# Kernel optimization log

Hardware: AMD Instinct MI355X
Metric: run time of the kernel (lower is better)

Reference implementation:

```python
import jax, jax.numpy as jnp
import numpy as np

BATCH, SEQ, DIM = 4, 4096, 256
DT_RANK, D_STATE, NUM_TOKENS = 16, 16, 1024


def _adapool(x, T):
    # uniform window mean == AdaptiveAvgPool1d when S % T == 0
    B, S, D = x.shape
    return x.reshape(B, T, S // T, D).mean(axis=2)


def _layernorm(x, g, b, eps=1e-5):
    mu = x.mean(-1, keepdims=True)
    var = ((x - mu) ** 2).mean(-1, keepdims=True)
    return (x - mu) * jax.lax.rsqrt(var + eps) * g + b


def _gauss_mask(T):
    c = (T + 1) // 2
    idx = jnp.arange(T, dtype=jnp.float32)
    sigma = jnp.abs(idx - c).mean()
    w = jnp.exp(-0.5 * (idx - c) ** 2 / sigma ** 2)
    return w / w.sum()


def _ssm(x, Wdbc, Wdt, bdt, Alog, D):
    A = -jnp.exp(Alog)                                     # (Dm, N)
    dbc = x @ Wdbc.T                                       # (B,L,dt+2N)
    delta = jax.nn.softplus(dbc[..., :DT_RANK] @ Wdt.T + bdt)   # (B,L,Dm)
    Bm = dbc[..., DT_RANK:DT_RANK + D_STATE]               # (B,L,N)
    Cm = dbc[..., DT_RANK + D_STATE:]                      # (B,L,N)
    deltaA = jnp.exp(delta[..., None] * A)                 # (B,L,Dm,N)
    BX = (delta[..., None] * Bm[:, :, None, :]) * x[..., None]
    def comb(c1, c2):
        a1, x1 = c1
        a2, x2 = c2
        return (a2 * a1, a2 * x1 + x2)
    _, hs = jax.lax.associative_scan(comb, (deltaA, BX), axis=1)
    y = jnp.einsum('bldn,bln->bld', hs, Cm) + D * x
    return y


def setup_inputs():
    key = jax.random.key(0)
    ks = jax.random.split(key, 16)
    s = 0.05
    Alog = jnp.tile(jnp.log(jnp.arange(1.0, D_STATE + 1.0, dtype=jnp.float32))[None, :], (DIM, 1))
    return {
        'x': jax.random.normal(ks[0], (BATCH, SEQ, DIM), jnp.float32),
        'ln_g': jnp.ones((DIM,), jnp.float32),
        'ln_b': jnp.zeros((DIM,), jnp.float32),
        'W1': jax.random.normal(ks[1], (DIM, DIM), jnp.float32) * s,
        'b1': jnp.zeros((DIM,), jnp.float32),
        'W2': jax.random.normal(ks[2], (DIM, DIM), jnp.float32) * s,
        'b2': jnp.zeros((DIM,), jnp.float32),
        'Wcf': jax.random.normal(ks[3], (DIM, DIM), jnp.float32) * s,
        'bcf': jnp.zeros((DIM,), jnp.float32),
        'Wcb': jax.random.normal(ks[4], (DIM, DIM), jnp.float32) * s,
        'bcb': jnp.zeros((DIM,), jnp.float32),
        'Wdbc_f': jax.random.normal(ks[5], (DT_RANK + 2 * D_STATE, DIM), jnp.float32) * s,
        'Wdt_f': jax.random.normal(ks[6], (DIM, DT_RANK), jnp.float32) * s,
        'bdt_f': jnp.zeros((DIM,), jnp.float32),
        'Alog_f': Alog,
        'D_f': jnp.ones((DIM,), jnp.float32),
        'Wdbc_b': jax.random.normal(ks[7], (DT_RANK + 2 * D_STATE, DIM), jnp.float32) * s,
        'Wdt_b': jax.random.normal(ks[8], (DIM, DT_RANK), jnp.float32) * s,
        'bdt_b': jnp.zeros((DIM,), jnp.float32),
        'Alog_b': Alog,
        'D_b': jnp.ones((DIM,), jnp.float32),
    }


def reference(x, ln_g, ln_b, W1, b1, W2, b2, Wcf, bcf, Wcb, bcb,
              Wdbc_f, Wdt_f, bdt_f, Alog_f, D_f,
              Wdbc_b, Wdt_b, bdt_b, Alog_b, D_b):
    skip = _adapool(x, NUM_TOKENS)
    xn = _layernorm(x, ln_g, ln_b)
    z = xn @ W1.T + b1
    xp = xn @ W2.T + b2
    mask = _gauss_mask(NUM_TOKENS)[None, :, None]

    # forward direction: 1x1 conv (= channel linear) -> softplus -> SSM
    h1 = jax.nn.softplus(jnp.einsum('bsd,ed->bse', xp, Wcf) + bcf)
    x1 = _ssm(h1, Wdbc_f, Wdt_f, bdt_f, Alog_f, D_f)
    x1 = jax.nn.silu(_adapool(x1, NUM_TOKENS) * mask)

    # backward direction on flipped sequence
    h2 = jax.nn.softplus(jnp.einsum('bsd,ed->bse', xp[:, ::-1], Wcb) + bcb)
    x2 = _ssm(h2, Wdbc_b, Wdt_b, bdt_b, Alog_b, D_b)[:, ::-1]
    x2 = jax.nn.silu(_adapool(x2, NUM_TOKENS) * mask)

    zp = jax.nn.silu(_adapool(z, NUM_TOKENS))
    return zp * x1 + zp * x2 + skip
```

## Files before the change

### kernel.cpp

```cpp
#include <hip/hip_runtime.h>
#include <math.h>


namespace {
constexpr int BB = 4;
constexpr int LL = 4096;
constexpr int DD = 256;
constexpr int NS = 16;
constexpr int NCH = 128;
constexpr int CLEN = 32;
constexpr int NG  = CLEN / 8;
constexpr int TOK = 1024;

constexpr size_t NROW = (size_t)BB * LL;
constexpr size_t NE   = NROW * DD;
constexpr size_t NP   = (size_t)BB * TOK * DD;
constexpr size_t NBC  = NROW * NS;
constexpr size_t NAGG = 2ull * BB * DD * NCH * NS;
constexpr size_t NSD  = 2ull * BB * NCH * DD;

constexpr size_t O_H1X  = 0;
constexpr size_t O_G2X  = NE / 2;
constexpr size_t O_H1T  = NE;
constexpr size_t O_G2T  = NE + NE / 2;
constexpr size_t O_DLTF = 2 * NE;
constexpr size_t O_XN   = O_DLTF;
constexpr size_t O_DLTB = 2 * NE + NE / 2;
constexpr size_t O_BMF  = 3 * NE;
constexpr size_t O_CMF  = O_BMF + NBC / 2;
constexpr size_t O_BMB  = O_CMF + NBC / 2;
constexpr size_t O_CMB  = O_BMB + NBC / 2;
constexpr size_t O_ZP   = O_CMB + NBC / 2;
constexpr size_t O_WF1  = O_ZP + NP;
constexpr size_t O_BF1  = O_WF1 + 768 * 256 / 2;
constexpr size_t O_WF2F = O_BF1 + 768;
constexpr size_t O_B2F  = O_WF2F + 384 * 256 / 2;
constexpr size_t O_WF2B = O_B2F + 384;
constexpr size_t O_B2B  = O_WF2B + 384 * 256 / 2;
constexpr size_t O_SD   = O_B2B + 384;
constexpr size_t O_HEND = O_SD + NSD;
constexpr size_t O_HIN  = O_HEND + NAGG / 2;
constexpr size_t O_MASK = O_HIN + NAGG / 2;

constexpr int SST = 136;
}

typedef __bf16 bf16x8 __attribute__((ext_vector_type(8)));
typedef __bf16 bf16x4 __attribute__((ext_vector_type(4)));
typedef float f32x4 __attribute__((ext_vector_type(4)));

__device__ __forceinline__ float softplusf(float x) {
    return fmaxf(x, 0.f) + __logf(1.f + __expf(-fabsf(x)));
}
__device__ __forceinline__ float siluf(float x) {
    return x / (1.f + __expf(-x));
}
__device__ __forceinline__ void gl_lds16(const void* g, void* l) {
    __builtin_amdgcn_global_load_lds((const __attribute__((address_space(1))) unsigned int*)g,
                                     (__attribute__((address_space(3))) unsigned int*)l, 16, 0, 0);
}
__device__ __forceinline__ int st_addr(int col, int row) {
    return col * SST + ((((row >> 3) ^ (col >> 3)) & 15) << 3) + (row & 7);
}
__device__ __forceinline__ void pow_chain(float e1, float* p) {
    p[0] = e1;
    p[1] = e1 * e1;
    p[2] = p[1] * e1;
    p[3] = p[1] * p[1];
    p[4] = p[3] * p[0];
    p[5] = p[3] * p[1];
    p[6] = p[3] * p[2];
    p[7] = p[3] * p[3];
    p[8]  = p[7] * p[0];
    p[9]  = p[7] * p[1];
    p[10] = p[7] * p[2];
    p[11] = p[7] * p[3];
    p[12] = p[7] * p[4];
    p[13] = p[7] * p[5];
    p[14] = p[7] * p[6];
    p[15] = p[7] * p[7];
}

#define GEMM_KLOOP(SHBASE, GA, GB, WR, WC, WV, LANE, ACC)                          \
    {                                                                               \
        _Pragma("unroll")                                                           \
        for (int rg = 0; rg < 2; ++rg) {                                            \
            gl_lds16((GA) + rg * 16 * 256, &(SHBASE)[((WV) * 2 + rg) * 512]);       \
            gl_lds16((GB) + rg * 16 * 256, &(SHBASE)[4096 + ((WV) * 2 + rg) * 512]);\
        }                                                                           \
        _Pragma("unroll")                                                           \
        for (int kst = 0; kst < 8; ++kst) {                                         \
            if (kst < 7) {                                                          \
                __bf16* Asn = (SHBASE) + ((kst + 1) & 1) * 8192;                    \
                int k0n = (kst + 1) * 32;                                           \
                _Pragma("unroll")                                                   \
                for (int rg = 0; rg < 2; ++rg) {                                    \
                    gl_lds16((GA) + rg * 16 * 256 + k0n, &Asn[((WV) * 2 + rg) * 512]);      \
                    gl_lds16((GB) + rg * 16 * 256 + k0n, &Asn[4096 + ((WV) * 2 + rg) * 512]);\
                }                                                                   \
                asm volatile("s_waitcnt vmcnt(4)" ::: "memory");                    \
            } else {                                                                \
                asm volatile("s_waitcnt vmcnt(0)" ::: "memory");                    \
            }                                                                       \
            __builtin_amdgcn_s_barrier();                                           \
            __builtin_amdgcn_sched_barrier(0);                                      \
            const __bf16* Ac = (SHBASE) + (kst & 1) * 8192;                         \
            const __bf16* Bc = Ac + 4096;                                           \
            bf16x8 af[4], bfr[4];                                                   \
            _Pragma("unroll")                                                       \
            for (int i = 0; i < 4; ++i)                                             \
                af[i] = *(const bf16x8*)&Ac[((WR) * 4 + i) * 512 + (LANE) * 8];     \
            _Pragma("unroll")                                                       \
            for (int j = 0; j < 4; ++j)                                             \
                bfr[j] = *(const bf16x8*)&Bc[((WC) * 4 + j) * 512 + (LANE) * 8];    \
            _Pragma("unroll")                                                       \
            for (int i = 0; i < 4; ++i)                                             \
                _Pragma("unroll")                                                   \
                for (int j = 0; j < 4; ++j)                                         \
                    ACC[i][j] = __builtin_amdgcn_mfma_f32_16x16x32_bf16(af[i], bfr[j], ACC[i][j], 0, 0, 0); \
            __builtin_amdgcn_s_barrier();                                           \
        }                                                                           \
    }

__global__ __launch_bounds__(256) void prep_ln_kernel(
    const float* __restrict__ x, const float* __restrict__ lng, const float* __restrict__ lnb,
    const float* __restrict__ W1, const float* __restrict__ b1,
    const float* __restrict__ W2, const float* __restrict__ b2,
    const float* __restrict__ Wcf, const float* __restrict__ bcf,
    const float* __restrict__ Wcb, const float* __restrict__ bcb,
    const float* __restrict__ Wdt_f, const float* __restrict__ Wdbc_f, const float* __restrict__ bdt_f,
    const float* __restrict__ Wdt_b, const float* __restrict__ Wdbc_b, const float* __restrict__ bdt_b,
    __bf16* __restrict__ xn, float* __restrict__ outp,
    __bf16* __restrict__ Wf1, float* __restrict__ bf1,
    __bf16* __restrict__ Wf2f, float* __restrict__ b2f,
    __bf16* __restrict__ Wf2b, float* __restrict__ b2b,
    float* __restrict__ mask)
{
    int bxg = blockIdx.x;
    int k = threadIdx.x;
    if (bxg < 4096) {
        __shared__ float red[32];
        __shared__ float mv[8];
        int t = k;
        int r0 = bxg * 4;
        float gg = lng[t], bbv = lnb[t];
        float v[4], s[4], q[4];
#pragma unroll
        for (int i = 0; i < 4; ++i) {
            v[i] = x[(size_t)(r0 + i) * 256 + t];
            s[i] = v[i];
            q[i] = v[i] * v[i];
        }
        for (int o = 32; o > 0; o >>= 1) {
#pragma unroll
            for (int i = 0; i < 4; ++i) {
                s[i] += __shfl_xor(s[i], o, 64);
                q[i] += __shfl_xor(q[i], o, 64);
            }
        }
        if ((t & 63) == 0) {
            int w = t >> 6;
#pragma unroll
            for (int i = 0; i < 4; ++i) { red[i * 4 + w] = s[i]; red[16 + i * 4 + w] = q[i]; }
        }
        __syncthreads();
        if (t < 4) {
            float S = red[t * 4 + 0] + red[t * 4 + 1] + red[t * 4 + 2] + red[t * 4 + 3];
            float Q = red[16 + t * 4 + 0] + red[16 + t * 4 + 1] + red[16 + t * 4 + 2] + red[16 + t * 4 + 3];
            float mu = S * (1.f / 256.f);
            mv[t * 2] = mu;
            mv[t * 2 + 1] = rsqrtf(Q * (1.f / 256.f) - mu * mu + 1e-5f);
        }
        __syncthreads();
        float acc = 0.f;
#pragma unroll
        for (int i = 0; i < 4; ++i) {
            xn[(size_t)(r0 + i) * 256 + t] = (__bf16)((v[i] - mv[i * 2]) * mv[i * 2 + 1] * gg + bbv);
            acc += v[i];
        }
        int b = r0 >> 12;
        int g = (r0 & 4095) >> 2;
        outp[((size_t)b * TOK + g) * 256 + t] = acc * 0.25f;
        return;
    }
    int j2 = bxg - 4096;
    int mat = j2 / 641;
    int bx = j2 % 641;
    if (bx < 256) {
        int j = bx;
        const float* Wc = mat ? Wcb : Wcf;
        float acc = 0.f, accb = 0.f;
#pragma unroll 8
        for (int m = 0; m < 256; ++m) {
            float w = Wc[j * 256 + m];
            acc  = fmaf(w, W2[m * 256 + k], acc);
            accb = fmaf(w, b2[m], accb);
        }
        Wf1[(size_t)(256 + mat * 256 + j) * 256 + k] = (__bf16)acc;
        if (k == 0) bf1[256 + mat * 256 + j] = accb + (mat ? bcb[j] : bcf[j]);
        if (mat == 0) {
            Wf1[(size_t)j * 256 + k] = (__bf16)W1[j * 256 + k];
            if (k == 0) bf1[j] = b1[j];
        }
    } else if (bx < 640) {
        int j = bx - 256;
        const float* Wdt  = mat ? Wdt_b : Wdt_f;
        const float* Wdbc = mat ? Wdbc_b : Wdbc_f;
        const float* bdt  = mat ? bdt_b : bdt_f;
        __bf16* Wf2 = mat ? Wf2b : Wf2f;
        float* b2x  = mat ? b2b : b2f;
        float val;
        if (j < 256) {
            float acc = 0.f;
#pragma unroll
            for (int m = 0; m < 16; ++m)
                acc = fmaf(Wdt[j * 16 + m], Wdbc[m * 256 + k], acc);
            val = acc;
        } else if (j < 288) {
            val = Wdbc[(16 + (j - 256)) * 256 + k];
        } else {
            val = 0.f;
        }
        Wf2[(size_t)j * 256 + k] = (__bf16)val;
        if (k == 0) b2x[j] = (j < 256) ? bdt[j] : 0.f;
    } else if (mat == 0) {
        __shared__ float red2[4];
        __shared__ float sb;
        float w[4];
        float loc = 0.f;
#pragma unroll
        for (int q = 0; q < 4; ++q) {
            float dd = (float)(k + 256 * q) - 512.f;
            w[q] = __expf(-0.5f * dd * dd * (1.f / 65536.f));
            loc += w[q];
        }
        for (int o = 32; o > 0; o >>= 1) loc += __shfl_xor(loc, o, 64);
        if ((k & 63) == 0) red2[k >> 6] = loc;
        __syncthreads();
        if (k == 0) sb = red2[0] + red2[1] + red2[2] + red2[3];
        __syncthreads();
        float inv = 1.f / sb;
#pragma unroll
        for (int q = 0; q < 4; ++q) mask[k + 256 * q] = w[q] * inv;
    }
}

__global__ __launch_bounds__(256) void gemm1_mfma(
    const __bf16* __restrict__ A, const __bf16* __restrict__ Bw, const float* __restrict__ bias,
    float* __restrict__ zp, __bf16* __restrict__ h1x, __bf16* __restrict__ g2x,
    __bf16* __restrict__ h1T, __bf16* __restrict__ g2T)
{
    __shared__ __align__(16) __bf16 SH[128 * SST];
    int tid = threadIdx.x;
    int lane = tid & 63, wv = tid >> 6;
    int wr = wv >> 1, wc = wv & 1;
    int lm = lane & 15, lq = lane >> 4;
    int m0 = blockIdx.x << 7, n0 = blockIdx.y << 7;

    const __bf16* gaB = A  + (size_t)(m0 + wv * 32 + lm) * 256 + lq * 8;
    const __bf16* gbB = Bw + (size_t)(n0 + wv * 32 + lm) * 256 + lq * 8;

    f32x4 acc[4][4];
#pragma unroll
    for (int i = 0; i < 4; ++i)
#pragma unroll
        for (int j = 0; j < 4; ++j) acc[i][j] = 0;

    GEMM_KLOOP(SH, gaB, gbB, wr, wc, wv, lane, acc)

    int target = blockIdx.y >> 1;
    int colbase = (blockIdx.y & 1) * 128;
    __syncthreads();
    if (target == 0) {
        float* zs = (float*)SH;
#pragma unroll
        for (int j = 0; j < 4; ++j) {
            int coll = wc * 64 + j * 16 + lm;
            float bv = bias[n0 + coll];
#pragma unroll
            for (int i = 0; i < 4; ++i) {
                int gl = wr * 16 + i * 4 + lq;
                float s = acc[i][j][0] + acc[i][j][1] + acc[i][j][2] + acc[i][j][3];
                zs[gl * 132 + coll] = siluf(0.25f * s + bv);
            }
        }
        __syncthreads();
        int b = m0 >> 12, g0 = (m0 & 4095) >> 2;
        int rl = tid >> 5;
        int c4 = (tid & 31) * 4;
#pragma unroll
        for (int p = 0; p < 4; ++p) {
            int g = p * 8 + rl;
            float4 v = *(float4*)&zs[g * 132 + c4];
            *(float4*)&zp[((size_t)b * TOK + g0 + g) * 256 + colbase + c4] = v;
        }
    } else {
        __bf16* hs = SH;
#pragma unroll
        for (int j = 0; j < 4; ++j) {
            int coll = wc * 64 + j * 16 + lm;
            float bv = bias[n0 + coll];
#pragma unroll
            for (int i = 0; i < 4; ++i) {
                int rl = wr * 64 + i * 16 + lq * 4;
                bf16x4 v4;
#pragma unroll
                for (int r = 0; r < 4; ++r)
                    v4[r] = (__bf16)softplusf(acc[i][j][r] + bv);
                *(bf16x4*)&hs[st_addr(coll, rl)] = v4;
            }
        }
        __syncthreads();
        __bf16* outp = (target == 1) ? h1x : g2x;
        __bf16* outT = (target == 1) ? h1T : g2T;
        {
            int tg = tid >> 4;
#pragma unroll
            for (int it = 0; it < 8; ++it) {
                int dcol = it * 16 + (tid & 15);
                bf16x8 v = *(const bf16x8*)&hs[dcol * SST + (((tg ^ (dcol >> 3)) & 15) << 3)];
                *(bf16x8*)&outT[(((size_t)(m0 >> 3) + tg) * 256 + colbase + dcol) * 8] = v;
            }
        }
        {
            int rl2 = tid >> 4;
            int c8 = (tid & 15) * 8;
#pragma unroll
            for (int p = 0; p < 8; ++p) {
                int row = p * 16 + rl2;
                bf16x8 v;
#pragma unroll
                for (int e = 0; e < 8; ++e) v[e] = hs[st_addr(c8 + e, row)];
                *(bf16x8*)&outp[(size_t)(m0 + row) * 256 + colbase + c8] = v;
            }
        }
    }
}

__global__ __launch_bounds__(256) void gemm2_mfma(
    const __bf16* __restrict__ h1x, const __bf16* __restrict__ g2x,
    const __bf16* __restrict__ Wf, const float* __restrict__ bf2,
    const __bf16* __restrict__ Wb, const float* __restrict__ bb2,
    __bf16* __restrict__ dTf, __bf16* __restrict__ dTb,
    __bf16* __restrict__ BmF, __bf16* __restrict__ CmF,
    __bf16* __restrict__ BmB, __bf16* __restrict__ CmB)
{
    __shared__ __align__(16) __bf16 SH[128 * SST];
    int tid = threadIdx.x;
    int lane = tid & 63, wv = tid >> 6;
    int wr = wv >> 1, wc = wv & 1;
    int lm = lane & 15, lq = lane >> 4;
    int m0 = blockIdx.x << 7, n0 = blockIdx.y << 7;
    int dir = blockIdx.z;
    const __bf16* A    = dir ? g2x : h1x;
    const __bf16* Bw   = dir ? Wb : Wf;
    const float* bias  = dir ? bb2 : bf2;
    __bf16* dT = dir ? dTb : dTf;
    __bf16* Bm = dir ? BmB : BmF;
    __bf16* Cm = dir ? CmB : CmF;

    const __bf16* gaB = A  + (size_t)(m0 + wv * 32 + lm) * 256 + lq * 8;
    const __bf16* gbB = Bw + (size_t)(n0 + wv * 32 + lm) * 256 + lq * 8;

    f32x4 acc[4][4];
#pragma unroll
    for (int i = 0; i < 4; ++i)
#pragma unroll
        for (int j = 0; j < 4; ++j) acc[i][j] = 0;

    GEMM_KLOOP(SH, gaB, gbB, wr, wc, wv, lane, acc)

    __syncthreads();
    if (blockIdx.y < 2) {
        __bf16* hs = SH;
        int colbase = blockIdx.y * 128;
#pragma unroll
        for (int j = 0; j < 4; ++j) {
            int coll = wc * 64 + j * 16 + lm;
            float bv = bias[n0 + coll];
#pragma unroll
            for (int i = 0; i < 4; ++i) {
                int rl = wr * 64 + i * 16 + lq * 4;
                bf16x4 v4;
#pragma unroll
                for (int r = 0; r < 4; ++r)
                    v4[r] = (__bf16)softplusf(acc[i][j][r] + bv);
                *(bf16x4*)&hs[st_addr(coll, rl)] = v4;
            }
        }
        __syncthreads();
        int tg = tid >> 4;
#pragma unroll
        for (int it = 0; it < 8; ++it) {
            int dcol = it * 16 + (tid & 15);
            bf16x8 v = *(const bf16x8*)&hs[dcol * SST + (((tg ^ (dcol >> 3)) & 15) << 3)];
            *(bf16x8*)&dT[(((size_t)(m0 >> 3) + tg) * 256 + colbase + dcol) * 8] = v;
        }
    } else {
        __bf16* bs_ = SH;
        __bf16* cs_ = SH + 128 * 24;
        if (wc == 0) {
#pragma unroll
            for (int j = 0; j < 2; ++j) {
                int coll = j * 16 + lm;
                float bv = bias[n0 + coll];
                __bf16* dst = j ? cs_ : bs_;
#pragma unroll
                for (int i = 0; i < 4; ++i) {
                    int rl = wr * 64 + i * 16 + lq * 4;
#pragma unroll
                    for (int r = 0; r < 4; ++r)
                        dst[(rl + r) * 24 + lm] = (__bf16)(acc[i][j][r] + bv);
                }
            }
        }
        __syncthreads();
        int row = tid >> 1;
        int c8 = (tid & 1) * 8;
        bf16x8 vb = *(bf16x8*)&bs_[row * 24 + c8];
        bf16x8 vc = *(bf16x8*)&cs_[row * 24 + c8];
        *(bf16x8*)&Bm[(size_t)(m0 + row) * 16 + c8] = vb;
        *(bf16x8*)&Cm[(size_t)(m0 + row) * 16 + c8] = vc;
    }
}

__global__ __launch_bounds__(256) void scan1_kernel(
    const __bf16* __restrict__ dTf, const __bf16* __restrict__ dTb,
    const __bf16* __restrict__ xTf, const __bf16* __restrict__ xTb,
    const __bf16* __restrict__ bmf, const __bf16* __restrict__ bmb,
    const float* __restrict__ alogf, const float* __restrict__ alogb,
    float* __restrict__ sdb, __bf16* __restrict__ hend)
{
    int d = threadIdx.x;
    int c = blockIdx.x, b = blockIdx.y, dir = blockIdx.z;
    const __bf16* dT = dir ? dTb : dTf;
    const __bf16* xT = dir ? xTb : xTf;
    const __bf16* Bm = dir ? bmb : bmf;
    const float* Alog = dir ? alogb : alogf;

    float A[16];
    bool intOK = true;
#pragma unroll
    for (int n = 0; n < 16; ++n) {
        A[n] = -__expf(Alog[(size_t)d * 16 + n]);
        intOK = intOK && (fabsf(A[n] + (float)(n + 1)) < 1e-3f);
    }
    float h[16];
#pragma unroll
    for (int n = 0; n < 16; ++n) h[n] = 0.f;
    float sd = 0.f;
    size_t rg0 = (size_t)b * 512 + (size_t)c * NG;
    size_t rowb = (size_t)b * LL + (size_t)c * CLEN;
    if (intOK) {
        for (int g = 0; g < NG; ++g) {
            int gg = dir ? (NG - 1 - g) : g;
            size_t ti = ((rg0 + gg) * 256 + d) * 8;
            bf16x8 dv = *(const bf16x8*)&dT[ti];
            bf16x8 xv8 = *(const bf16x8*)&xT[ti];
#pragma unroll
            for (int ii = 0; ii < 8; ++ii) {
                int i = dir ? (7 - ii) : ii;
                float dlt = (float)dv[i];
                float xv  = (float)xv8[i];
                float common = dlt * xv;
                sd += dlt;
                float p[16];
                pow_chain(__expf(-dlt), p);
                const bf16x8* Bp = (const bf16x8*)&Bm[(rowb + gg * 8 + i) * NS];
                bf16x8 b0 = Bp[0], b1 = Bp[1];
#pragma unroll
                for (int n = 0; n < 8; ++n) {
                    h[n]     = fmaf(p[n],     h[n],     common * (float)b0[n]);
                    h[n + 8] = fmaf(p[n + 8], h[n + 8], common * (float)b1[n]);
                }
            }
        }
    } else {
        for (int g = 0; g < NG; ++g) {
            int gg = dir ? (NG - 1 - g) : g;
            size_t ti = ((rg0 + gg) * 256 + d) * 8;
            bf16x8 dv = *(const bf16x8*)&dT[ti];
            bf16x8 xv8 = *(const bf16x8*)&xT[ti];
#pragma unroll
            for (int ii = 0; ii < 8; ++ii) {
                int i = dir ? (7 - ii) : ii;
                float dlt = (float)dv[i];
                float xv  = (float)xv8[i];
                float common = dlt * xv;
                sd += dlt;
                const bf16x8* Bp = (const bf16x8*)&Bm[(rowb + gg * 8 + i) * NS];
                bf16x8 b0 = Bp[0], b1 = Bp[1];
#pragma unroll
                for (int n = 0; n < 8; ++n) {
                    h[n]     = fmaf(__expf(dlt * A[n]),     h[n],     common * (float)b0[n]);
                    h[n + 8] = fmaf(__expf(dlt * A[n + 8]), h[n + 8], common * (float)b1[n]);
                }
            }
        }
    }
    size_t sbase = (size_t)(dir * 4 + b) * NCH + c;
    sdb[sbase * 256 + d] = sd;
    size_t hb = sbase * 16 * 256 + d;
#pragma unroll
    for (int n = 0; n < 16; ++n) hend[hb + (size_t)n * 256] = (__bf16)h[n];
}

__global__ __launch_bounds__(128) void scan2_kernel(
    const float* __restrict__ sdb, const __bf16* __restrict__ hend,
    const float* __restrict__ alogf, const float* __restrict__ alogb,
    __bf16* __restrict__ hin)
{
    int blk = blockIdx.x >> 1;
    int n = blk & 15, b = (blk >> 4) & 3, dir = blk >> 6;
    int d = ((blockIdx.x & 1) << 7) + threadIdx.x;
    const float* Alog = dir ? alogb : alogf;
    float A_dn = -__expf(Alog[(size_t)d * 16 + n]);
    size_t basec = (size_t)(dir * 4 + b) * NCH;
    float s = 0.f;
    if (!dir) {
#pragma unroll 8
        for (int c = 0; c < NCH; ++c) {
            float sdv = sdb[(basec + c) * 256 + d];
            size_t idx = ((basec + c) * 16 + n) * 256 + d;
            float he = (float)hend[idx];
            hin[idx] = (__bf16)s;
            s = fmaf(__expf(sdv * A_dn), s, he);
        }
    } else {
#pragma unroll 8
        for (int c = NCH - 1; c >= 0; --c) {
            float sdv = sdb[(basec + c) * 256 + d];
            size_t idx = ((basec + c) * 16 + n) * 256 + d;
            float he = (float)hend[idx];
            hin[idx] = (__bf16)s;
            s = fmaf(__expf(sdv * A_dn), s, he);
        }
    }
}

__global__ __launch_bounds__(256) void scan3_kernel(
    const __bf16* __restrict__ dTf, const __bf16* __restrict__ dTb,
    const __bf16* __restrict__ xTf, const __bf16* __restrict__ xTb,
    const __bf16* __restrict__ bmf, const __bf16* __restrict__ bmb,
    const __bf16* __restrict__ cmf, const __bf16* __restrict__ cmb,
    const float* __restrict__ alogf, const float* __restrict__ alogb,
    const float* __restrict__ Dfp, const float* __restrict__ Dbp,
    const __bf16* __restrict__ hin,
    const float* __restrict__ zp, const float* __restrict__ mask,
    float* __restrict__ outp)
{
    int d = threadIdx.x;
    int c = blockIdx.x, b = blockIdx.y, dir = blockIdx.z;
    const __bf16* dT = dir ? dTb : dTf;
    const __bf16* xT = dir ? xTb : xTf;
    const __bf16* Bm = dir ? bmb : bmf;
    const __bf16* Cm = dir ? cmb : cmf;
    const float* Alog = dir ? alogb : alogf;
    const float* Dv   = dir ? Dbp : Dfp;

    float A[16];
    bool intOK = true;
#pragma unroll
    for (int n = 0; n < 16; ++n) {
        A[n] = -__expf(Alog[(size_t)d * 16 + n]);
        intOK = intOK && (fabsf(A[n] + (float)(n + 1)) < 1e-3f);
    }
    float Dd = Dv[d];
    float h[16];
    size_t hb = ((size_t)(dir * 4 + b) * NCH + c) * 16 * 256 + d;
#pragma unroll
    for (int n = 0; n < 16; ++n) h[n] = (float)hin[hb + (size_t)n * 256];

    size_t rg0 = (size_t)b * 512 + (size_t)c * NG;
    size_t rowb = (size_t)b * LL + (size_t)c * CLEN;
    int base = c * CLEN;
    float pool = 0.f;
    if (intOK) {
        for (int g = 0; g < NG; ++g) {
            int gg = dir ? (NG - 1 - g) : g;
            size_t ti = ((rg0 + gg) * 256 + d) * 8;
            bf16x8 dv = *(const bf16x8*)&dT[ti];
            bf16x8 xv8 = *(const bf16x8*)&xT[ti];
#pragma unroll
            for (int ii = 0; ii < 8; ++ii) {
                int i = dir ? (7 - ii) : ii;
                float dlt = (float)dv[i];
                float xv  = (float)xv8[i];
                float common = dlt * xv;
                float p[16];
                pow_chain(__expf(-dlt), p);
                size_t row = rowb + gg * 8 + i;
                const bf16x8* Bp = (const bf16x8*)&Bm[row * NS];
                const bf16x8* Cp = (const bf16x8*)&Cm[row * NS];
                bf16x8 b0 = Bp[0], b1 = Bp[1];
                bf16x8 c0 = Cp[0], c1 = Cp[1];
                float yac = 0.f;
#pragma unroll
                for (int n = 0; n < 8; ++n) {
                    h[n]     = fmaf(p[n],     h[n],     common * (float)b0[n]);
                    h[n + 8] = fmaf(p[n + 8], h[n + 8], common * (float)b1[n]);
                    yac = fmaf(h[n], (float)c0[n], yac);
                    yac = fmaf(h[n + 8], (float)c1[n], yac);
                }
                pool += yac + Dd * xv;
                int t = base + gg * 8 + i;
                bool gend = dir ? ((t & 3) == 0) : ((t & 3) == 3);
                if (gend) {
                    int gtok = t >> 2;
                    size_t ip = ((size_t)b * TOK + gtok) * 256 + d;
                    float contrib = zp[ip] * siluf(pool * 0.25f * mask[gtok]);
                    atomicAdd(&outp[ip], contrib);
                    pool = 0.f;
                }
            }
        }
    } else {
        for (int g = 0; g < NG; ++g) {
            int gg = dir ? (NG - 1 - g) : g;
            size_t ti = ((rg0 + gg) * 256 + d) * 8;
            bf16x8 dv = *(const bf16x8*)&dT[ti];
            bf16x8 xv8 = *(const bf16x8*)&xT[ti];
#pragma unroll
            for (int ii = 0; ii < 8; ++ii) {
                int i = dir ? (7 - ii) : ii;
                float dlt = (float)dv[i];
                float xv  = (float)xv8[i];
                float common = dlt * xv;
                size_t row = rowb + gg * 8 + i;
                const bf16x8* Bp = (const bf16x8*)&Bm[row * NS];
                const bf16x8* Cp = (const bf16x8*)&Cm[row * NS];
                bf16x8 b0 = Bp[0], b1 = Bp[1];
                bf16x8 c0 = Cp[0], c1 = Cp[1];
                float yac = 0.f;
#pragma unroll
                for (int n = 0; n < 8; ++n) {
                    h[n]     = fmaf(__expf(dlt * A[n]),     h[n],     common * (float)b0[n]);
                    h[n + 8] = fmaf(__expf(dlt * A[n + 8]), h[n + 8], common * (float)b1[n]);
                    yac = fmaf(h[n], (float)c0[n], yac);
                    yac = fmaf(h[n + 8], (float)c1[n], yac);
                }
                pool += yac + Dd * xv;
                int t = base + gg * 8 + i;
                bool gend = dir ? ((t & 3) == 0) : ((t & 3) == 3);
                if (gend) {
                    int gtok = t >> 2;
                    size_t ip = ((size_t)b * TOK + gtok) * 256 + d;
                    float contrib = zp[ip] * siluf(pool * 0.25f * mask[gtok]);
                    atomicAdd(&outp[ip], contrib);
                    pool = 0.f;
                }
            }
        }
    }
}

extern "C" void kernel_launch(void* const* d_in, const int* in_sizes, int n_in,
                              void* d_out, int out_size, void* d_ws, size_t ws_size,
                              hipStream_t stream)
{
    const float* x      = (const float*)d_in[0];
    const float* ln_g   = (const float*)d_in[1];
    const float* ln_b   = (const float*)d_in[2];
    const float* W1     = (const float*)d_in[3];
    const float* b1     = (const float*)d_in[4];
    const float* W2     = (const float*)d_in[5];
    const float* b2     = (const float*)d_in[6];
    const float* Wcf    = (const float*)d_in[7];
    const float* bcf    = (const float*)d_in[8];
    const float* Wcb    = (const float*)d_in[9];
    const float* bcb    = (const float*)d_in[10];
    const float* Wdbc_f = (const float*)d_in[11];
    const float* Wdt_f  = (const float*)d_in[12];
    const float* bdt_f  = (const float*)d_in[13];
    const float* Alog_f = (const float*)d_in[14];
    const float* D_f    = (const float*)d_in[15];
    const float* Wdbc_b = (const float*)d_in[16];
    const float* Wdt_b  = (const float*)d_in[17];
    const float* bdt_b  = (const float*)d_in[18];
    const float* Alog_b = (const float*)d_in[19];
    const float* D_b    = (const float*)d_in[20];
    float* out = (float*)d_out;
    float* ws  = (float*)d_ws;

    __bf16* h1x = (__bf16*)(ws + O_H1X);
    __bf16* g2x = (__bf16*)(ws + O_G2X);
    __bf16* h1T = (__bf16*)(ws + O_H1T);
    __bf16* g2T = (__bf16*)(ws + O_G2T);
    __bf16* xnb = (__bf16*)(ws + O_XN);
    __bf16* dTf = (__bf16*)(ws + O_DLTF);
    __bf16* dTb = (__bf16*)(ws + O_DLTB);
    __bf16* bmf = (__bf16*)(ws + O_BMF);
    __bf16* cmf = (__bf16*)(ws + O_CMF);
    __bf16* bmb = (__bf16*)(ws + O_BMB);
    __bf16* cmb = (__bf16*)(ws + O_CMB);
    float* zpb  = ws + O_ZP;
    __bf16* wf1 = (__bf16*)(ws + O_WF1);
    float* bf1  = ws + O_BF1;
    __bf16* wf2f = (__bf16*)(ws + O_WF2F);
    float* b2f  = ws + O_B2F;
    __bf16* wf2b = (__bf16*)(ws + O_WF2B);
    float* b2b  = ws + O_B2B;
    float* sdb  = ws + O_SD;
    __bf16* hnd = (__bf16*)(ws + O_HEND);
    __bf16* hin = (__bf16*)(ws + O_HIN);
    float* mkb  = ws + O_MASK;

    prep_ln_kernel<<<dim3(4096 + 1282), 256, 0, stream>>>(
        x, ln_g, ln_b,
        W1, b1, W2, b2, Wcf, bcf, Wcb, bcb,
        Wdt_f, Wdbc_f, bdt_f, Wdt_b, Wdbc_b, bdt_b,
        xnb, out, wf1, bf1, wf2f, b2f, wf2b, b2b, mkb);
    gemm1_mfma<<<dim3(128, 6), 256, 0, stream>>>(xnb, wf1, bf1, zpb, h1x, g2x, h1T, g2T);
    gemm2_mfma<<<dim3(128, 3, 2), 256, 0, stream>>>(h1x, g2x, wf2f, b2f, wf2b, b2b,
                                                    dTf, dTb, bmf, cmf, bmb, cmb);
    scan1_kernel<<<dim3(NCH, BB, 2), 256, 0, stream>>>(dTf, dTb, h1T, g2T, bmf, bmb,
                                                       Alog_f, Alog_b, sdb, hnd);
    scan2_kernel<<<256, 128, 0, stream>>>(sdb, hnd, Alog_f, Alog_b, hin);
    scan3_kernel<<<dim3(NCH, BB, 2), 256, 0, stream>>>(dTf, dTb, h1T, g2T, bmf, bmb, cmf, cmb,
                                                       Alog_f, Alog_b, D_f, D_b, hin,
                                                       zpb, mkb, out);
}
```

Measured before the change: 213.1 us.

## Merge scan3 directions per block and replace atomics with shared-memory reduction

scan3 now runs both scan directions in a single 512-thread block for each chunk. Each thread writes its pooled contribution to shared memory, then one pass adds both directions into the output with plain read-add-write, replacing per-element atomicAdd. Separately, the prep kernel's fused-weight product now computes 8 output rows per block with register accumulation and a warp-shuffle reduction for the bias, which shrinks the grid. The risks are a larger block and shared-memory footprint in scan3, and it only stays correct because each chunk maps to exactly its own 8 tokens.

```diff
diff --git a/kernel.cpp b/kernel.cpp
--- a/kernel.cpp
+++ b/kernel.cpp
@@ -184,26 +184,52 @@
         return;
     }
     int j2 = bxg - 4096;
-    int mat = j2 / 641;
-    int bx = j2 % 641;
-    if (bx < 256) {
-        int j = bx;
-        const float* Wc = mat ? Wcb : Wcf;
-        float acc = 0.f, accb = 0.f;
-#pragma unroll 8
+    int mat = j2 / 417;
+    int bx = j2 % 417;
+    if (bx < 32) {
+        int j0 = bx * 8;
+        const float* Wc  = mat ? Wcb : Wcf;
+        const float* bcx = mat ? bcb : bcf;
+        float b2v = b2[k];
+        float acc[8];
+#pragma unroll
+        for (int jj = 0; jj < 8; ++jj) acc[jj] = 0.f;
+#pragma unroll 4
         for (int m = 0; m < 256; ++m) {
-            float w = Wc[j * 256 + m];
-            acc  = fmaf(w, W2[m * 256 + k], acc);
-            accb = fmaf(w, b2[m], accb);
-        }
-        Wf1[(size_t)(256 + mat * 256 + j) * 256 + k] = (__bf16)acc;
-        if (k == 0) bf1[256 + mat * 256 + j] = accb + (mat ? bcb[j] : bcf[j]);
+            float w2v = W2[m * 256 + k];
+#pragma unroll
+            for (int jj = 0; jj < 8; ++jj)
+                acc[jj] = fmaf(Wc[(j0 + jj) * 256 + m], w2v, acc[jj]);
+        }
+#pragma unroll
+        for (int jj = 0; jj < 8; ++jj)
+            Wf1[(size_t)(256 + mat * 256 + j0 + jj) * 256 + k] = (__bf16)acc[jj];
+        __shared__ float redb[32];
+        float pb[8];
+#pragma unroll
+        for (int jj = 0; jj < 8; ++jj) pb[jj] = Wc[(j0 + jj) * 256 + k] * b2v;
+        for (int o = 32; o > 0; o >>= 1) {
+#pragma unroll
+            for (int jj = 0; jj < 8; ++jj) pb[jj] += __shfl_xor(pb[jj], o, 64);
+        }
+        if ((k & 63) == 0) {
+            int w = k >> 6;
+#pragma unroll
+            for (int jj = 0; jj < 8; ++jj) redb[jj * 4 + w] = pb[jj];
+        }
+        __syncthreads();
+        if (k < 8) {
+            float s = redb[k * 4] + redb[k * 4 + 1] + redb[k * 4 + 2] + redb[k * 4 + 3];
+            bf1[256 + mat * 256 + j0 + k] = s + bcx[j0 + k];
+        }
         if (mat == 0) {
-            Wf1[(size_t)j * 256 + k] = (__bf16)W1[j * 256 + k];
-            if (k == 0) bf1[j] = b1[j];
-        }
-    } else if (bx < 640) {
-        int j = bx - 256;
+#pragma unroll
+            for (int jj = 0; jj < 8; ++jj)
+                Wf1[(size_t)(j0 + jj) * 256 + k] = (__bf16)W1[(j0 + jj) * 256 + k];
+            if (k < 8) bf1[j0 + k] = b1[j0 + k];
+        }
+    } else if (bx < 416) {
+        int j = bx - 32;
         const float* Wdt  = mat ? Wdt_b : Wdt_f;
         const float* Wdbc = mat ? Wdbc_b : Wdbc_f;
         const float* bdt  = mat ? bdt_b : bdt_f;
@@ -538,7 +564,7 @@
     }
 }
 
-__global__ __launch_bounds__(256) void scan3_kernel(
+__global__ __launch_bounds__(512) void scan3_kernel(
     const __bf16* __restrict__ dTf, const __bf16* __restrict__ dTb,
     const __bf16* __restrict__ xTf, const __bf16* __restrict__ xTb,
     const __bf16* __restrict__ bmf, const __bf16* __restrict__ bmb,
@@ -549,8 +575,11 @@
     const float* __restrict__ zp, const float* __restrict__ mask,
     float* __restrict__ outp)
 {
-    int d = threadIdx.x;
-    int c = blockIdx.x, b = blockIdx.y, dir = blockIdx.z;
+    __shared__ float ls[4096];
+    int tid = threadIdx.x;
+    int d = tid & 255;
+    int dir = tid >> 8;
+    int c = blockIdx.x, b = blockIdx.y;
     const __bf16* dT = dir ? dTb : dTf;
     const __bf16* xT = dir ? xTb : xTf;
     const __bf16* Bm = dir ? bmb : bmf;
@@ -607,9 +636,9 @@
                 bool gend = dir ? ((t & 3) == 0) : ((t & 3) == 3);
                 if (gend) {
                     int gtok = t >> 2;
+                    int gl = gtok - (c << 3);
                     size_t ip = ((size_t)b * TOK + gtok) * 256 + d;
-                    float contrib = zp[ip] * siluf(pool * 0.25f * mask[gtok]);
-                    atomicAdd(&outp[ip], contrib);
+                    ls[(dir << 11) + (gl << 8) + d] = zp[ip] * siluf(pool * 0.25f * mask[gtok]);
                     pool = 0.f;
                 }
             }
@@ -644,13 +673,21 @@
                 bool gend = dir ? ((t & 3) == 0) : ((t & 3) == 3);
                 if (gend) {
                     int gtok = t >> 2;
+                    int gl = gtok - (c << 3);
                     size_t ip = ((size_t)b * TOK + gtok) * 256 + d;
-                    float contrib = zp[ip] * siluf(pool * 0.25f * mask[gtok]);
-                    atomicAdd(&outp[ip], contrib);
+                    ls[(dir << 11) + (gl << 8) + d] = zp[ip] * siluf(pool * 0.25f * mask[gtok]);
                     pool = 0.f;
                 }
             }
         }
+    }
+    __syncthreads();
+    if (tid < 256) {
+        int gtok0 = c << 3;
+        size_t ipb = ((size_t)b * TOK + gtok0) * 256 + tid;
+#pragma unroll
+        for (int gl = 0; gl < 8; ++gl)
+            outp[ipb + (size_t)gl * 256] += ls[(gl << 8) + tid] + ls[2048 + (gl << 8) + tid];
     }
 }
 
@@ -705,7 +742,7 @@
     __bf16* hin = (__bf16*)(ws + O_HIN);
     float* mkb  = ws + O_MASK;
 
-    prep_ln_kernel<<<dim3(4096 + 1282), 256, 0, stream>>>(
+    prep_ln_kernel<<<dim3(4096 + 834), 256, 0, stream>>>(
         x, ln_g, ln_b,
         W1, b1, W2, b2, Wcf, bcf, Wcb, bcb,
         Wdt_f, Wdbc_f, bdt_f, Wdt_b, Wdbc_b, bdt_b,
@@ -716,7 +753,7 @@
     scan1_kernel<<<dim3(NCH, BB, 2), 256, 0, stream>>>(dTf, dTb, h1T, g2T, bmf, bmb,
                                                        Alog_f, Alog_b, sdb, hnd);
     scan2_kernel<<<256, 128, 0, stream>>>(sdb, hnd, Alog_f, Alog_b, hin);
-    scan3_kernel<<<dim3(NCH, BB, 2), 256, 0, stream>>>(dTf, dTb, h1T, g2T, bmf, bmb, cmf, cmb,
-                                                       Alog_f, Alog_b, D_f, D_b, hin,
-                                                       zpb, mkb, out);
-}
+    scan3_kernel<<<dim3(NCH, BB), 512, 0, stream>>>(dTf, dTb, h1T, g2T, bmf, bmb, cmf, cmb,
+                                                    Alog_f, Alog_b, D_f, D_b, hin,
+                                                    zpb, mkb, out);
+}
```

Result: slower. 233.5 us (+9.6%).
